# Kernel optimization log

Hardware: AMD Instinct MI355X
Metric: run time of the kernel (lower is better)

Reference implementation:

```python
import jax, jax.numpy as jnp
import numpy as np

DIM = 1024
NUM_HEADS = 16
HEAD_DIM = DIM // NUM_HEADS
SCALE = float(np.sqrt(HEAD_DIM))
NEG = -1e9


def setup_inputs() -> dict:
    key = jax.random.key(0)
    ks = jax.random.split(key, 12)
    B, S = 2, 2048
    std = 1.0 / np.sqrt(DIM)
    inp = {
        'query': jax.random.normal(ks[0], (B, S, DIM), jnp.float32),
        'key': jax.random.normal(ks[1], (B, S, DIM), jnp.float32),
        'value': jax.random.normal(ks[2], (B, S, DIM), jnp.float32),
        'key_padding_mask': jnp.ones((B, S), jnp.int32),
        'Wq': jax.random.normal(ks[3], (DIM, DIM), jnp.float32) * std,
        'bq': jax.random.normal(ks[4], (DIM,), jnp.float32) * std,
        'Wk': jax.random.normal(ks[5], (DIM, DIM), jnp.float32) * std,
        'bk': jax.random.normal(ks[6], (DIM,), jnp.float32) * std,
        'Wv': jax.random.normal(ks[7], (DIM, DIM), jnp.float32) * std,
        'bv': jax.random.normal(ks[8], (DIM,), jnp.float32) * std,
        'Wo': jax.random.normal(ks[9], (DIM, DIM), jnp.float32) * std,
        'bo': jax.random.normal(ks[10], (DIM,), jnp.float32) * std,
    }
    return inp


def reference(query, key, value, key_padding_mask, Wq, bq, Wk, bk, Wv, bv, Wo, bo):
    B, S, _ = query.shape
    # QKV projections (torch Linear: x @ W.T + b), split heads -> [B,H,S,D]
    def proj(x, W, b):
        return (x @ W.T + b).reshape(B, -1, NUM_HEADS, HEAD_DIM).transpose(0, 2, 1, 3)
    Q = proj(query, Wq, bq)
    K = proj(key, Wk, bk)
    V = proj(value, Wv, bv)
    # scaled dot-product scores [B,H,Sq,Sk]
    scores = jnp.einsum('bhqd,bhkd->bhqk', Q, K) / SCALE
    # key padding mask: positions where mask == 0 are filled with -1e9
    pad = (key_padding_mask == 0)[:, None, None, :]  # [B,1,1,Sk]
    scores = jnp.where(pad, NEG, scores)
    attention_weights = jax.nn.softmax(scores, axis=-1)
    context = jnp.einsum('bhqk,bhkd->bhqd', attention_weights, V)
    context = context.transpose(0, 2, 1, 3).reshape(B, -1, DIM)
    out = context @ Wo.T + bo
    return out, attention_weights
```

## Files before the change

### kernel.cpp

```cpp
#include <hip/hip_runtime.h>
#include <hip/hip_bf16.h>
#include <stdint.h>

#define DIMM 1024
#define HEADS 16
#define HD 64
#define BB 2
#define SS 2048
#define NTOK (BB*SS)

typedef __attribute__((ext_vector_type(8))) __bf16 bf16x8;
typedef __attribute__((ext_vector_type(4))) __bf16 bf16x4;
typedef __attribute__((ext_vector_type(4))) float f32x4;

__device__ __forceinline__ f32x4 mfma16(bf16x8 a, bf16x8 b, f32x4 c) {
  return __builtin_amdgcn_mfma_f32_16x16x32_bf16(a, b, c, 0, 0, 0);
}

__device__ __forceinline__ void gload_lds16(const void* g, void* l) {
  __builtin_amdgcn_global_load_lds(
      (__attribute__((address_space(1))) void*)(void*)g,
      (__attribute__((address_space(3))) void*)l,
      16, 0, 0);
}

#define LOG2E 1.4426950408889634f
#define C2 (0.125f * LOG2E)
#define NBRAW (-8e9f)

struct CvtArgs {
  const float* src[7];
  __bf16* dst[7];
  int n[7];
};

__global__ __launch_bounds__(256) void cvt_kernel(CvtArgs a) {
  const int t = blockIdx.y;
  const long i = ((long)blockIdx.x * 256 + threadIdx.x) * 8;
  if (i >= a.n[t]) return;
  const float* s = a.src[t] + i;
  f32x4 x0 = *(const f32x4*)s;
  f32x4 x1 = *(const f32x4*)(s + 4);
  bf16x8 o;
  o[0] = (__bf16)x0[0]; o[1] = (__bf16)x0[1]; o[2] = (__bf16)x0[2]; o[3] = (__bf16)x0[3];
  o[4] = (__bf16)x1[0]; o[5] = (__bf16)x1[1]; o[6] = (__bf16)x1[2]; o[7] = (__bf16)x1[3];
  *(bf16x8*)(a.dst[t] + i) = o;
}

__global__ void maskbits_kernel(const int* __restrict__ msk, uint32_t* __restrict__ mbits) {
  int j = threadIdx.x;
  if (j >= 128) return;
  const int* src = msk + j * 32;
  uint32_t wdd = 0;
#pragma unroll
  for (int i = 0; i < 32; ++i) wdd |= (src[i] != 0 ? 1u : 0u) << i;
  mbits[j] = wdd;
}

struct GemmArgs {
  const __bf16* A[3];
  const __bf16* B[3];
  const float* bias[3];
  void* out[3];
  int mode[3];
};

__global__ __launch_bounds__(256) void gemm_bt(GemmArgs ga) {
  const int z = blockIdx.z;
  const __bf16* __restrict__ A  = ga.A[z];
  const __bf16* __restrict__ Bm = ga.B[z];
  const float* __restrict__ bias = ga.bias[z];
  void* Cout = ga.out[z];
  const int mode = ga.mode[z];

  __shared__ __align__(16) char sA[2][16384];
  __shared__ __align__(16) char sB[2][16384];
  const int tid = threadIdx.x;
  const int w = tid >> 6, l = tid & 63;
  const int wr = w >> 1, wc = w & 1;
  const int lg = l >> 4, lr = l & 15;
  const int m0 = blockIdx.y * 128, n0 = blockIdx.x * 128;

  f32x4 acc[4][4] = {};

  auto stage = [&](int k0, int buf) {
#pragma unroll
    for (int i = 0; i < 4; ++i) {
      int c = (i * 4 + w) * 64 + l;
      int row = c >> 3, ch = c & 7;
      gload_lds16(A + (size_t)(m0 + row) * 1024 + k0 + ((ch ^ (row & 7)) << 3),
                  &sA[buf][(i * 4 + w) * 1024]);
    }
#pragma unroll
    for (int i = 0; i < 4; ++i) {
      int c = (i * 4 + w) * 64 + l;
      int row = c >> 3, ch = c & 7;
      gload_lds16(Bm + (size_t)(n0 + row) * 1024 + k0 + ((ch ^ (row & 7)) << 3),
                  &sB[buf][(i * 4 + w) * 1024]);
    }
  };

  stage(0, 0);
  __syncthreads();

  for (int ks = 0; ks < 16; ++ks) {
    const int cur = ks & 1;
    if (ks < 15) stage((ks + 1) * 64, cur ^ 1);
#pragma unroll
    for (int kk = 0; kk < 2; ++kk) {
      bf16x8 af[4], bfv[4];
#pragma unroll
      for (int fm = 0; fm < 4; ++fm) {
        int row = wr * 64 + fm * 16 + lr;
        af[fm] = *(const bf16x8*)&sA[cur][row * 128 + (((kk * 4 + lg) ^ (row & 7)) << 4)];
      }
#pragma unroll
      for (int fn = 0; fn < 4; ++fn) {
        int row = wc * 64 + fn * 16 + lr;
        bfv[fn] = *(const bf16x8*)&sB[cur][row * 128 + (((kk * 4 + lg) ^ (row & 7)) << 4)];
      }
#pragma unroll
      for (int fm = 0; fm < 4; ++fm)
#pragma unroll
        for (int fn = 0; fn < 4; ++fn)
          acc[fm][fn] = mfma16(af[fm], bfv[fn], acc[fm][fn]);
    }
    __syncthreads();
  }

#pragma unroll
  for (int fm = 0; fm < 4; ++fm) {
#pragma unroll
    for (int fn = 0; fn < 4; ++fn) {
      const int n = n0 + wc * 64 + fn * 16 + lr;
      const int mb = m0 + wr * 64 + fm * 16 + 4 * lg;
      const float bval = bias[n];
      f32x4 vv = acc[fm][fn];
      if (mode == 2) {
        float* C = (float*)Cout;
#pragma unroll
        for (int r = 0; r < 4; ++r)
          C[(size_t)(mb + r) * 1024 + n] = vv[r] + bval;
      } else if (mode == 0) {
        __bf16* C = (__bf16*)Cout;
        const int hh = n >> 6, d = n & 63;
#pragma unroll
        for (int r = 0; r < 4; ++r) {
          int m = mb + r;
          C[(((size_t)(m >> 11) * 16 + hh) * 2048 + (m & 2047)) * 64 + d] =
              (__bf16)(vv[r] + bval);
        }
      } else {
        __bf16* C = (__bf16*)Cout;
        const int hh = n >> 6, d = n & 63;
        bf16x4 pk;
#pragma unroll
        for (int r = 0; r < 4; ++r) pk[r] = (__bf16)(vv[r] + bval);
        *(bf16x4*)(C + (((size_t)(mb >> 11) * 16 + hh) * 64 + d) * 2048 + (mb & 2047)) = pk;
      }
    }
  }
}

__global__ __launch_bounds__(256) void attn_kernel(
    const __bf16* __restrict__ Qh, const __bf16* __restrict__ Kh,
    const __bf16* __restrict__ Vt, const uint32_t* __restrict__ mbits,
    float* __restrict__ attnW, __bf16* __restrict__ ctx)
{
  __shared__ __align__(16) char sK[2][8192];
  __shared__ __align__(16) char sV[2][8192];
  __shared__ __align__(16) __bf16 sPB[4][16][64];

  const int tid = threadIdx.x;
  const int w = tid >> 6, l = tid & 63;
  const int lg = l >> 4, lr = l & 15;

  const int bid = blockIdx.x;
  const int xcd = bid & 7, j = bid >> 3;
  const int bh = xcd * 4 + (j >> 5);
  const int q0 = (j & 31) * 64;
  const int b = bh >> 4, h = bh & 15;

  const __bf16* qbase = Qh + ((size_t)bh * SS + q0 + w * 16 + lr) * HD;
  bf16x8 qf0 = *(const bf16x8*)(qbase + lg * 8);
  bf16x8 qf1 = *(const bf16x8*)(qbase + 32 + lg * 8);

  const __bf16* Khead = Kh + (size_t)bh * SS * HD;
  const __bf16* Vhead = Vt + (size_t)bh * HD * SS;
  const uint32_t* mrow = mbits + b * 64;

  const int c0 = w * 64 + l;

  auto stageK = [&](int k0, int buf) {
#pragma unroll
    for (int i = 0; i < 2; ++i) {
      int c = i * 256 + c0;
      int kr = c >> 3, ch = c & 7;
      gload_lds16(Khead + (size_t)(k0 + kr) * HD + ((ch ^ (kr & 7)) << 3),
                  &sK[buf][(i * 4 + w) * 1024]);
    }
  };
  auto stageV = [&](int k0, int buf) {
#pragma unroll
    for (int i = 0; i < 2; ++i) {
      int c = i * 256 + c0;
      int d = c >> 3, ch = c & 7;
      gload_lds16(Vhead + (size_t)d * SS + k0 + ((ch ^ (d & 7)) << 3),
                  &sV[buf][(i * 4 + w) * 1024]);
    }
  };

  stageK(0, 0);
  asm volatile("s_waitcnt vmcnt(0)" ::: "memory");
  __builtin_amdgcn_s_barrier();

  float lsum = 0.0f;

  for (int t = 0; t < 32; ++t) {
    const int cur = t & 1;
    if (t < 31) stageK((t + 1) * 64, cur ^ 1);

    const uint32_t mw0 = mrow[2 * t], mw1 = mrow[2 * t + 1];
    const bool fast = ((mw0 & mw1) == 0xFFFFFFFFu);

#pragma unroll
    for (int sub = 0; sub < 4; ++sub) {
      const int kr = sub * 16 + lr;
      bf16x8 k0f = *(const bf16x8*)&sK[cur][kr * 128 + ((lg ^ (kr & 7)) << 4)];
      bf16x8 k1f = *(const bf16x8*)&sK[cur][kr * 128 + (((4 + lg) ^ (kr & 7)) << 4)];
      __builtin_amdgcn_s_setprio(1);
      f32x4 a = {};
      a = mfma16(k0f, qf0, a);
      a = mfma16(k1f, qf1, a);
      __builtin_amdgcn_s_setprio(0);
      if (!fast) {
        uint32_t bits = ((sub < 2) ? mw0 : mw1) >> ((sub & 1) * 16 + 4 * lg);
#pragma unroll
        for (int r = 0; r < 4; ++r) a[r] = ((bits >> r) & 1) ? a[r] : NBRAW;
      }
#pragma unroll
      for (int r = 0; r < 4; ++r)
        lsum += __builtin_amdgcn_exp2f(fminf(a[r] * C2, 80.0f));
    }
    asm volatile("s_waitcnt vmcnt(0)" ::: "memory");
    __builtin_amdgcn_s_barrier();
  }

  lsum += __shfl_xor(lsum, 16);
  lsum += __shfl_xor(lsum, 32);
  const float rl = 1.0f / lsum;

  f32x4 Oa[4] = {};
  float* pwbase = attnW + ((size_t)bh * SS + q0 + w * 16) * SS;

  stageK(0, 0);
  stageV(0, 0);
  asm volatile("s_waitcnt vmcnt(0)" ::: "memory");
  __builtin_amdgcn_s_barrier();

  for (int t = 0; t < 32; ++t) {
    const int cur = t & 1;
    if (t < 31) { stageK((t + 1) * 64, cur ^ 1); stageV((t + 1) * 64, cur ^ 1); }

    const uint32_t mw0 = mrow[2 * t], mw1 = mrow[2 * t + 1];
    const bool fast = ((mw0 & mw1) == 0xFFFFFFFFu);

#pragma unroll
    for (int sub = 0; sub < 4; ++sub) {
      const int kr = sub * 16 + lr;
      bf16x8 k0f = *(const bf16x8*)&sK[cur][kr * 128 + ((lg ^ (kr & 7)) << 4)];
      bf16x8 k1f = *(const bf16x8*)&sK[cur][kr * 128 + (((4 + lg) ^ (kr & 7)) << 4)];
      __builtin_amdgcn_s_setprio(1);
      f32x4 a = {};
      a = mfma16(k0f, qf0, a);
      a = mfma16(k1f, qf1, a);
      __builtin_amdgcn_s_setprio(0);
      if (!fast) {
        uint32_t bits = ((sub < 2) ? mw0 : mw1) >> ((sub & 1) * 16 + 4 * lg);
#pragma unroll
        for (int r = 0; r < 4; ++r) a[r] = ((bits >> r) & 1) ? a[r] : NBRAW;
      }
      bf16x4 pk;
#pragma unroll
      for (int r = 0; r < 4; ++r)
        pk[r] = (__bf16)(__builtin_amdgcn_exp2f(fminf(a[r] * C2, 80.0f)) * rl);
      const int cc = ((sub * 2 + (lg >> 1)) ^ (lr & 7));
      *(bf16x4*)((char*)&sPB[w][lr][0] + cc * 16 + (lg & 1) * 8) = pk;
    }

#pragma unroll
    for (int i = 0; i < 4; ++i) {
      const int row = i * 4 + (l >> 4);
      const int jj = l & 15;
      const int cc = (jj >> 1) ^ (row & 7);
      bf16x4 pb = *(const bf16x4*)((const char*)&sPB[w][row][0] + cc * 16 + (jj & 1) * 8);
      f32x4 pv;
#pragma unroll
      for (int r = 0; r < 4; ++r) pv[r] = (float)pb[r];
      __builtin_nontemporal_store(pv,
          (f32x4*)(pwbase + (size_t)row * SS + t * 64 + jj * 4));
    }

#pragma unroll
    for (int hh = 0; hh < 2; ++hh) {
      bf16x8 pa = *(const bf16x8*)((const char*)&sPB[w][lr][0] +
                                   (((hh * 4 + lg) ^ (lr & 7)) * 16));
      __builtin_amdgcn_s_setprio(1);
#pragma unroll
      for (int dg = 0; dg < 4; ++dg) {
        const int d = dg * 16 + lr;
        bf16x8 vb = *(const bf16x8*)&sV[cur][d * 128 + (((hh * 4 + lg) ^ (d & 7)) << 4)];
        Oa[dg] = mfma16(pa, vb, Oa[dg]);
      }
      __builtin_amdgcn_s_setprio(0);
    }

    asm volatile("s_waitcnt vmcnt(4)" ::: "memory");
    __builtin_amdgcn_s_barrier();
  }

#pragma unroll
  for (int dg = 0; dg < 4; ++dg)
#pragma unroll
    for (int r = 0; r < 4; ++r)
      ctx[(size_t)(b * SS + q0 + w * 16 + 4 * lg + r) * DIMM + h * HD + dg * 16 + lr] =
          (__bf16)Oa[dg][r];
}

extern "C" void kernel_launch(void* const* d_in, const int* in_sizes, int n_in,
                              void* d_out, int out_size, void* d_ws, size_t ws_size,
                              hipStream_t stream)
{
  const float* q   = (const float*)d_in[0];
  const float* k   = (const float*)d_in[1];
  const float* v   = (const float*)d_in[2];
  const int*   msk = (const int*)d_in[3];
  const float* Wq  = (const float*)d_in[4];
  const float* bq  = (const float*)d_in[5];
  const float* Wk  = (const float*)d_in[6];
  const float* bk  = (const float*)d_in[7];
  const float* Wv  = (const float*)d_in[8];
  const float* bv  = (const float*)d_in[9];
  const float* Wo  = (const float*)d_in[10];
  const float* bo  = (const float*)d_in[11];

  char* ws = (char*)d_ws;
  __bf16* xq  = (__bf16*)(ws);
  __bf16* xk  = (__bf16*)(ws + (8u << 20));
  __bf16* xv  = (__bf16*)(ws + (16u << 20));
  __bf16* wqb = (__bf16*)(ws + (24u << 20));
  __bf16* wkb = (__bf16*)(ws + (26u << 20));
  __bf16* wvb = (__bf16*)(ws + (28u << 20));
  __bf16* wob = (__bf16*)(ws + (30u << 20));
  __bf16* Qh  = (__bf16*)(ws + (32u << 20));
  __bf16* Kh  = (__bf16*)(ws + (40u << 20));
  __bf16* Vt  = (__bf16*)(ws + (48u << 20));
  __bf16* ctx = (__bf16*)(ws + (56u << 20));
  uint32_t* mbits = (uint32_t*)(ws + (64u << 20));

  CvtArgs ca;
  ca.src[0] = q;  ca.dst[0] = xq;  ca.n[0] = NTOK * DIMM;
  ca.src[1] = k;  ca.dst[1] = xk;  ca.n[1] = NTOK * DIMM;
  ca.src[2] = v;  ca.dst[2] = xv;  ca.n[2] = NTOK * DIMM;
  ca.src[3] = Wq; ca.dst[3] = wqb; ca.n[3] = DIMM * DIMM;
  ca.src[4] = Wk; ca.dst[4] = wkb; ca.n[4] = DIMM * DIMM;
  ca.src[5] = Wv; ca.dst[5] = wvb; ca.n[5] = DIMM * DIMM;
  ca.src[6] = Wo; ca.dst[6] = wob; ca.n[6] = DIMM * DIMM;
  cvt_kernel<<<dim3(2048, 7, 1), 256, 0, stream>>>(ca);
  maskbits_kernel<<<1, 128, 0, stream>>>(msk, mbits);

  GemmArgs g1;
  g1.A[0] = xq; g1.B[0] = wqb; g1.bias[0] = bq; g1.out[0] = (void*)Qh; g1.mode[0] = 0;
  g1.A[1] = xk; g1.B[1] = wkb; g1.bias[1] = bk; g1.out[1] = (void*)Kh; g1.mode[1] = 0;
  g1.A[2] = xv; g1.B[2] = wvb; g1.bias[2] = bv; g1.out[2] = (void*)Vt; g1.mode[2] = 1;
  gemm_bt<<<dim3(8, 32, 3), 256, 0, stream>>>(g1);

  float* out = (float*)d_out;
  float* attnW = out + (size_t)NTOK * DIMM;
  attn_kernel<<<dim3(1024, 1, 1), 256, 0, stream>>>(Qh, Kh, Vt, mbits, attnW, ctx);

  GemmArgs g2;
  g2.A[0] = ctx; g2.B[0] = wob; g2.bias[0] = bo; g2.out[0] = (void*)out; g2.mode[0] = 2;
  g2.A[1] = ctx; g2.B[1] = wob; g2.bias[1] = bo; g2.out[1] = (void*)out; g2.mode[1] = 2;
  g2.A[2] = ctx; g2.B[2] = wob; g2.bias[2] = bo; g2.out[2] = (void*)out; g2.mode[2] = 2;
  gemm_bt<<<dim3(8, 32, 1), 256, 0, stream>>>(g2);
}
```

Before: 244.2 us.

## Fuse fp32-to-bf16 activation conversion into QKV GEMM A-tile loads

```diff
diff --git a/kernel.cpp b/kernel.cpp
--- a/kernel.cpp
+++ b/kernel.cpp
@@ -29,13 +29,25 @@
 #define NBRAW (-8e9f)
 
 struct CvtArgs {
-  const float* src[7];
-  __bf16* dst[7];
-  int n[7];
+  const float* src[4];
+  __bf16* dst[4];
+  int n[4];
+  const int* msk;
+  uint32_t* mbits;
 };
 
 __global__ __launch_bounds__(256) void cvt_kernel(CvtArgs a) {
   const int t = blockIdx.y;
+  if (t == 4) {
+    if (blockIdx.x == 0 && threadIdx.x < 128) {
+      const int* src = a.msk + threadIdx.x * 32;
+      uint32_t wdd = 0;
+#pragma unroll
+      for (int i = 0; i < 32; ++i) wdd |= (src[i] != 0 ? 1u : 0u) << i;
+      a.mbits[threadIdx.x] = wdd;
+    }
+    return;
+  }
   const long i = ((long)blockIdx.x * 256 + threadIdx.x) * 8;
   if (i >= a.n[t]) return;
   const float* s = a.src[t] + i;
@@ -47,18 +59,9 @@
   *(bf16x8*)(a.dst[t] + i) = o;
 }
 
-__global__ void maskbits_kernel(const int* __restrict__ msk, uint32_t* __restrict__ mbits) {
-  int j = threadIdx.x;
-  if (j >= 128) return;
-  const int* src = msk + j * 32;
-  uint32_t wdd = 0;
-#pragma unroll
-  for (int i = 0; i < 32; ++i) wdd |= (src[i] != 0 ? 1u : 0u) << i;
-  mbits[j] = wdd;
-}
-
 struct GemmArgs {
   const __bf16* A[3];
+  const float* Af[3];
   const __bf16* B[3];
   const float* bias[3];
   void* out[3];
@@ -68,6 +71,7 @@
 __global__ __launch_bounds__(256) void gemm_bt(GemmArgs ga) {
   const int z = blockIdx.z;
   const __bf16* __restrict__ A  = ga.A[z];
+  const float* __restrict__ Af  = ga.Af[z];
   const __bf16* __restrict__ Bm = ga.B[z];
   const float* __restrict__ bias = ga.bias[z];
   void* Cout = ga.out[z];
@@ -83,7 +87,7 @@
 
   f32x4 acc[4][4] = {};
 
-  auto stage = [&](int k0, int buf) {
+  auto stageA_g = [&](int k0, int buf) {
 #pragma unroll
     for (int i = 0; i < 4; ++i) {
       int c = (i * 4 + w) * 64 + l;
@@ -91,6 +95,8 @@
       gload_lds16(A + (size_t)(m0 + row) * 1024 + k0 + ((ch ^ (row & 7)) << 3),
                   &sA[buf][(i * 4 + w) * 1024]);
     }
+  };
+  auto stageB = [&](int k0, int buf) {
 #pragma unroll
     for (int i = 0; i < 4; ++i) {
       int c = (i * 4 + w) * 64 + l;
@@ -100,12 +106,42 @@
     }
   };
 
-  stage(0, 0);
+  if (Af) {
+#pragma unroll
+    for (int i = 0; i < 4; ++i) {
+      int c = (i * 4 + w) * 64 + l;
+      int row = c >> 3, ch = c & 7;
+      const float* src = Af + (size_t)(m0 + row) * 1024 + ((ch ^ (row & 7)) << 3);
+      f32x4 x0 = *(const f32x4*)src;
+      f32x4 x1 = *(const f32x4*)(src + 4);
+      bf16x8 o;
+#pragma unroll
+      for (int r = 0; r < 4; ++r) { o[r] = (__bf16)x0[r]; o[4 + r] = (__bf16)x1[r]; }
+      *(bf16x8*)&sA[0][c * 16] = o;
+    }
+  } else {
+    stageA_g(0, 0);
+  }
+  stageB(0, 0);
   __syncthreads();
 
   for (int ks = 0; ks < 16; ++ks) {
     const int cur = ks & 1;
-    if (ks < 15) stage((ks + 1) * 64, cur ^ 1);
+    f32x4 a0_[4], a1_[4];
+    if (Af && ks < 15) {
+#pragma unroll
+      for (int i = 0; i < 4; ++i) {
+        int c = (i * 4 + w) * 64 + l;
+        int row = c >> 3, ch = c & 7;
+        const float* src = Af + (size_t)(m0 + row) * 1024 + (ks + 1) * 64 +
+                           ((ch ^ (row & 7)) << 3);
+        a0_[i] = *(const f32x4*)src;
+        a1_[i] = *(const f32x4*)(src + 4);
+      }
+    }
+    if (!Af && ks < 15) stageA_g((ks + 1) * 64, cur ^ 1);
+    if (ks < 15) stageB((ks + 1) * 64, cur ^ 1);
+
 #pragma unroll
     for (int kk = 0; kk < 2; ++kk) {
       bf16x8 af[4], bfv[4];
@@ -124,6 +160,17 @@
 #pragma unroll
         for (int fn = 0; fn < 4; ++fn)
           acc[fm][fn] = mfma16(af[fm], bfv[fn], acc[fm][fn]);
+    }
+
+    if (Af && ks < 15) {
+#pragma unroll
+      for (int i = 0; i < 4; ++i) {
+        int c = (i * 4 + w) * 64 + l;
+        bf16x8 o;
+#pragma unroll
+        for (int r = 0; r < 4; ++r) { o[r] = (__bf16)a0_[i][r]; o[4 + r] = (__bf16)a1_[i][r]; }
+        *(bf16x8*)&sA[cur ^ 1][c * 16] = o;
+      }
     }
     __syncthreads();
   }
@@ -345,9 +392,6 @@
   const float* bo  = (const float*)d_in[11];
 
   char* ws = (char*)d_ws;
-  __bf16* xq  = (__bf16*)(ws);
-  __bf16* xk  = (__bf16*)(ws + (8u << 20));
-  __bf16* xv  = (__bf16*)(ws + (16u << 20));
   __bf16* wqb = (__bf16*)(ws + (24u << 20));
   __bf16* wkb = (__bf16*)(ws + (26u << 20));
   __bf16* wvb = (__bf16*)(ws + (28u << 20));
@@ -359,20 +403,17 @@
   uint32_t* mbits = (uint32_t*)(ws + (64u << 20));
 
   CvtArgs ca;
-  ca.src[0] = q;  ca.dst[0] = xq;  ca.n[0] = NTOK * DIMM;
-  ca.src[1] = k;  ca.dst[1] = xk;  ca.n[1] = NTOK * DIMM;
-  ca.src[2] = v;  ca.dst[2] = xv;  ca.n[2] = NTOK * DIMM;
-  ca.src[3] = Wq; ca.dst[3] = wqb; ca.n[3] = DIMM * DIMM;
-  ca.src[4] = Wk; ca.dst[4] = wkb; ca.n[4] = DIMM * DIMM;
-  ca.src[5] = Wv; ca.dst[5] = wvb; ca.n[5] = DIMM * DIMM;
-  ca.src[6] = Wo; ca.dst[6] = wob; ca.n[6] = DIMM * DIMM;
-  cvt_kernel<<<dim3(2048, 7, 1), 256, 0, stream>>>(ca);
-  maskbits_kernel<<<1, 128, 0, stream>>>(msk, mbits);
+  ca.src[0] = Wq; ca.dst[0] = wqb; ca.n[0] = DIMM * DIMM;
+  ca.src[1] = Wk; ca.dst[1] = wkb; ca.n[1] = DIMM * DIMM;
+  ca.src[2] = Wv; ca.dst[2] = wvb; ca.n[2] = DIMM * DIMM;
+  ca.src[3] = Wo; ca.dst[3] = wob; ca.n[3] = DIMM * DIMM;
+  ca.msk = msk; ca.mbits = mbits;
+  cvt_kernel<<<dim3(512, 5, 1), 256, 0, stream>>>(ca);
 
   GemmArgs g1;
-  g1.A[0] = xq; g1.B[0] = wqb; g1.bias[0] = bq; g1.out[0] = (void*)Qh; g1.mode[0] = 0;
-  g1.A[1] = xk; g1.B[1] = wkb; g1.bias[1] = bk; g1.out[1] = (void*)Kh; g1.mode[1] = 0;
-  g1.A[2] = xv; g1.B[2] = wvb; g1.bias[2] = bv; g1.out[2] = (void*)Vt; g1.mode[2] = 1;
+  g1.A[0] = nullptr; g1.Af[0] = q; g1.B[0] = wqb; g1.bias[0] = bq; g1.out[0] = (void*)Qh; g1.mode[0] = 0;
+  g1.A[1] = nullptr; g1.Af[1] = k; g1.B[1] = wkb; g1.bias[1] = bk; g1.out[1] = (void*)Kh; g1.mode[1] = 0;
+  g1.A[2] = nullptr; g1.Af[2] = v; g1.B[2] = wvb; g1.bias[2] = bv; g1.out[2] = (void*)Vt; g1.mode[2] = 1;
   gemm_bt<<<dim3(8, 32, 3), 256, 0, stream>>>(g1);
 
   float* out = (float*)d_out;
@@ -380,8 +421,8 @@
   attn_kernel<<<dim3(1024, 1, 1), 256, 0, stream>>>(Qh, Kh, Vt, mbits, attnW, ctx);
 
   GemmArgs g2;
-  g2.A[0] = ctx; g2.B[0] = wob; g2.bias[0] = bo; g2.out[0] = (void*)out; g2.mode[0] = 2;
-  g2.A[1] = ctx; g2.B[1] = wob; g2.bias[1] = bo; g2.out[1] = (void*)out; g2.mode[1] = 2;
-  g2.A[2] = ctx; g2.B[2] = wob; g2.bias[2] = bo; g2.out[2] = (void*)out; g2.mode[2] = 2;
+  g2.A[0] = ctx; g2.Af[0] = nullptr; g2.B[0] = wob; g2.bias[0] = bo; g2.out[0] = (void*)out; g2.mode[0] = 2;
+  g2.A[1] = ctx; g2.Af[1] = nullptr; g2.B[1] = wob; g2.bias[1] = bo; g2.out[1] = (void*)out; g2.mode[1] = 2;
+  g2.A[2] = ctx; g2.Af[2] = nullptr; g2.B[2] = wob; g2.bias[2] = bo; g2.out[2] = (void*)out; g2.mode[2] = 2;
   gemm_bt<<<dim3(8, 32, 1), 256, 0, stream>>>(g2);
 }
```

Result: slower. 253.4 us (+3.8%).
